# Kernel tuning notes

Hardware: AMD Instinct MI355X
Metric: run time of the kernel (lower is better)

Reference implementation:

```python
import jax, jax.numpy as jnp
import numpy as np

D_MODEL = 512
BINS = 64


def setup_inputs() -> dict:
    key = jax.random.key(0)
    ks = jax.random.split(key, 5)
    x = jax.random.normal(ks[0], (1, 512, D_MODEL), dtype=jnp.float32)
    # torch Linear(2d, d): weight [d, 2d]; store transposed [2d, d] for x @ W
    s1 = 1.0 / np.sqrt(2 * D_MODEL)
    W1 = jax.random.uniform(ks[1], (2 * D_MODEL, D_MODEL), jnp.float32, -s1, s1)
    b1 = jax.random.uniform(ks[2], (D_MODEL,), jnp.float32, -s1, s1)
    s2 = 1.0 / np.sqrt(D_MODEL)
    W2 = jax.random.uniform(ks[3], (D_MODEL, BINS), jnp.float32, -s2, s2)
    b2 = jax.random.uniform(ks[4], (BINS,), jnp.float32, -s2, s2)
    return {"x": x, "W1": W1, "b1": b1, "W2": W2, "b2": b2}


def reference(x, W1, b1, W2, b2):
    # pair = cat([xi, xj], -1); Linear(cat) == xi @ W1[:d] + xj @ W1[d:]
    # This factorization is exact and avoids materializing the [B,N,N,2d] tensor.
    d = x.shape[-1]
    hi = jnp.einsum('bnd,de->bne', x, W1[:d])      # [B, N, d]
    hj = jnp.einsum('bnd,de->bne', x, W1[d:])      # [B, N, d]
    h = hi[:, :, None, :] + hj[:, None, :, :] + b1  # [B, N, N, d]
    h = jax.nn.gelu(h, approximate=False)           # torch nn.GELU default is exact
    return jnp.einsum('bijd,de->bije', h, W2) + b2  # [B, N, N, bins]
```

## Files before the change

### kernel.cpp

```cpp
#include <hip/hip_runtime.h>
#include <hip/hip_fp16.h>

#define D 512
#define NTOK 512
#define BINS 64

typedef float v4f __attribute__((ext_vector_type(4)));
typedef int v4i __attribute__((ext_vector_type(4)));
typedef short short8 __attribute__((ext_vector_type(8)));
typedef _Float16 h8 __attribute__((ext_vector_type(8)));
typedef _Float16 h4 __attribute__((ext_vector_type(4)));

__device__ __forceinline__ __half2 gelu2(__half2 x) {
    __half2 a = __builtin_bit_cast(__half2, __builtin_bit_cast(int, x) & 0x7fff7fff);
    __half2 s = __hmul2(a, a);
    __half2 m = __hfma2(s, __float2half2_rn(-0.1029437f),
                           __float2half2_rn(-2.3022082f));
    __half2 q = __hmul2(a, m);
    __half2 e = h2exp2(q);
    __half2 n = __hfma2(e, __float2half2_rn(0.228584f),  __float2half2_rn(-0.675920f));
    n = __hfma2(e, n, __float2half2_rn(0.946902f));
    n = __hfma2(e, n, __float2half2_rn(-0.998521f));
    __half2 p = __hfma2(e, n, __float2half2_rn(1.0f));
    __half2 xneg = __hmul2(__hsub2(x, a), __float2half2_rn(0.5f));
    return __hfma2(a, p, xneg);
}

__device__ __forceinline__ __half2 bc_h2(int v) { return __builtin_bit_cast(__half2, v); }
__device__ __forceinline__ int bc_i(__half2 v) { return __builtin_bit_cast(int, v); }

__device__ __forceinline__ v4i pack8(v4f a, v4f b) {
    h8 o;
    o[0] = (_Float16)a.x; o[1] = (_Float16)a.y; o[2] = (_Float16)a.z; o[3] = (_Float16)a.w;
    o[4] = (_Float16)b.x; o[5] = (_Float16)b.y; o[6] = (_Float16)b.z; o[7] = (_Float16)b.w;
    return __builtin_bit_cast(v4i, o);
}

__global__ __launch_bounds__(256) void k_pack(const float* __restrict__ x,
                                              const float* __restrict__ W1,
                                              const float* __restrict__ W2,
                                              v4i* __restrict__ Ap,
                                              v4i* __restrict__ Wp,
                                              short8* __restrict__ Bp) {
    const int b = blockIdx.x;
    const int t = threadIdx.x;
    if (b < 32) {
        const int rb = b;
#pragma unroll
        for (int u = 0; u < 4; ++u) {
            const int e = t + 256 * u;
            const int l = e & 63, ks = e >> 6;
            const float* src = x + (size_t)(rb * 16 + (l & 15)) * D + ks * 32 + (l >> 4) * 8;
            v4f a = *(const v4f*)src;
            v4f c = *(const v4f*)(src + 4);
            Ap[(size_t)(rb * 16 + ks) * 64 + l] = pack8(a, c);
        }
    } else if (b < 288) {
        const int slot = (b - 32) * 256 + t;
        const int l = slot & 63;
        const int ks = (slot >> 6) & 15;
        const int nb = slot >> 10;
        const int ng = nb * 16 + (l & 15);
        const float* src = W1 + (size_t)((ng >> 9) * D + ks * 32 + (l >> 4) * 8) * D
                              + (ng & 511);
        h8 o;
#pragma unroll
        for (int j = 0; j < 8; ++j) o[j] = (_Float16)src[(size_t)j * D];
        Wp[(size_t)(nb * 16 + ks) * 64 + l] = __builtin_bit_cast(v4i, o);
    } else {
        const int tid = (b - 288) * 256 + t;
        const int ll = tid & 63;
        const int nt = (tid >> 6) & 3;
        const int kt = tid >> 8;
        const int colp = nt * 16 + (ll & 15);
        const int krow = kt * 32 + (ll >> 4) * 8;
        short8 v;
#pragma unroll
        for (int u = 0; u < 8; ++u) {
            _Float16 hv = (_Float16)W2[(size_t)(krow + u) * BINS + colp];
            v[u] = __builtin_bit_cast(short, hv);
        }
        Bp[tid] = v;
    }
}

__global__ __launch_bounds__(256) void k_gemm(const v4i* __restrict__ Ap,
                                              const v4i* __restrict__ Wp,
                                              const float* __restrict__ b1,
                                              _Float16* __restrict__ hi,
                                              _Float16* __restrict__ hj) {
    const int l = threadIdx.x & 63;
    const int w = threadIdx.x >> 6;
    const int c = l & 15;
    const int q = l >> 4;
    const int mb = blockIdx.x >> 4;
    const int cb = blockIdx.x & 15;
    const int nb = cb * 4 + w;

    const v4i* ap = Ap + (size_t)mb * 16 * 64 + l;
    const v4i* wp = Wp + (size_t)nb * 16 * 64 + l;

    v4f acc = {0.f, 0.f, 0.f, 0.f};
#pragma unroll 4
    for (int ks = 0; ks < 16; ++ks) {
        v4i a0 = ap[ks * 64];
        v4i bb = wp[ks * 64];
        acc = __builtin_amdgcn_mfma_f32_16x16x32_f16(__builtin_bit_cast(h8, a0),
                                                     __builtin_bit_cast(h8, bb), acc, 0, 0, 0);
    }

    const int ng = nb * 16 + c;
    const float b1v = (ng < D) ? b1[ng] : 0.0f;
    _Float16* dst = (ng < D ? hi : hj) + (ng & 511);
    const int row0 = mb * 16 + q * 4;
#pragma unroll
    for (int r = 0; r < 4; ++r)
        dst[(size_t)(row0 + r) * D] = (_Float16)(acc[r] + b1v);
}

__global__ __launch_bounds__(256, 6) void k_main(const __half* __restrict__ hi,
                                                 const __half* __restrict__ hj,
                                                 const v4i* __restrict__ Bp,
                                                 const float* __restrict__ b2,
                                                 float* __restrict__ out) {
    const int l = threadIdx.x & 63;
    const int w = threadIdx.x >> 6;
    const int c = l & 15;
    const int q = l >> 4;
    const int ib = (blockIdx.x >> 5) * 8;
    const int j0 = (blockIdx.x & 31) * 16;

    const __half* hjp = hj + (size_t)(j0 + c) * D + q * 8;
    const __half* hip = hi + (size_t)(ib + w * 2) * D + q * 8;
    const v4i* bp = Bp + l;

    v4f acc[2][4] = {};

    for (int kt = 0; kt < 16; ++kt) {
        const int ko = kt * 32;
        v4i hjraw = *(const v4i*)(hjp + ko);
        __half2 j0h = bc_h2(hjraw.x), j1h = bc_h2(hjraw.y);
        __half2 j2h = bc_h2(hjraw.z), j3h = bc_h2(hjraw.w);
        v4i bfr[4];
#pragma unroll
        for (int nt = 0; nt < 4; ++nt)
            bfr[nt] = bp[(kt * 4 + nt) * 64];
#pragma unroll
        for (int p = 0; p < 2; ++p) {
            v4i ar = *(const v4i*)(hip + (size_t)p * D + ko);
            __half2 g0 = gelu2(__hadd2(bc_h2(ar.x), j0h));
            __half2 g1 = gelu2(__hadd2(bc_h2(ar.y), j1h));
            __half2 g2 = gelu2(__hadd2(bc_h2(ar.z), j2h));
            __half2 g3 = gelu2(__hadd2(bc_h2(ar.w), j3h));
            v4i ai = {bc_i(g0), bc_i(g1), bc_i(g2), bc_i(g3)};
            h8 af = __builtin_bit_cast(h8, ai);
#pragma unroll
            for (int nt = 0; nt < 4; ++nt)
                acc[p][nt] = __builtin_amdgcn_mfma_f32_16x16x32_f16(
                    af, __builtin_bit_cast(h8, bfr[nt]), acc[p][nt], 0, 0, 0);
        }
    }

    const int i0 = ib + w * 2;
#pragma unroll
    for (int p = 0; p < 2; ++p) {
        const size_t rowbase = ((size_t)(i0 + p) * NTOK + j0 + q * 4) * BINS;
#pragma unroll
        for (int nt = 0; nt < 4; ++nt) {
            const float bb = b2[nt * 16 + c];
            float* op = out + rowbase + nt * 16 + c;
#pragma unroll
            for (int rr = 0; rr < 4; ++rr)
                op[(size_t)rr * BINS] = acc[p][nt][rr] + bb;
        }
    }
}

extern "C" void kernel_launch(void* const* d_in, const int* in_sizes, int n_in,
                              void* d_out, int out_size, void* d_ws, size_t ws_size,
                              hipStream_t stream) {
    const float* x  = (const float*)d_in[0];
    const float* W1 = (const float*)d_in[1];
    const float* b1 = (const float*)d_in[2];
    const float* W2 = (const float*)d_in[3];
    const float* b2 = (const float*)d_in[4];
    float* out = (float*)d_out;

    char* ws = (char*)d_ws;
    __half* hi = (__half*)ws;
    __half* hj = (__half*)(ws + (512u << 10));
    short8* Bp = (short8*)(ws + (1u << 20));
    v4i*    Ap = (v4i*)(ws + (1u << 20) + (64u << 10));
    v4i*    Wp = (v4i*)(ws + (1u << 20) + (64u << 10) + (512u << 10));

    k_pack<<<304, 256, 0, stream>>>(x, W1, W2, Ap, Wp, Bp);
    k_gemm<<<512, 256, 0, stream>>>(Ap, Wp, b1, (_Float16*)hi, (_Float16*)hj);
    k_main<<<2048, 256, 0, stream>>>(hi, hj, (const v4i*)Bp, b2, out);
}
```

Before: 132.1 us.

## Fuse pack and GEMM kernels, software-pipeline loads in main kernel

The separate fp16 packing kernel and the projection GEMM kernel are merged into one prep kernel. It reads x and W1 directly as fp32 and converts them in registers, while extra blocks pack W2. This removes one launch and the intermediate packed buffers. The main kernel now double-buffers its hj, hi and W2 fragment loads one k-step ahead, fully unrolls the loop, and lowers the launch-bounds occupancy hint from 6 to 3 to leave room for more registers. Risks are strided, uncoalesced W1 reads inside the GEMM and lower occupancy in the main kernel.

```diff
diff --git a/kernel.cpp b/kernel.cpp
--- a/kernel.cpp
+++ b/kernel.cpp
@@ -29,46 +29,17 @@
 __device__ __forceinline__ __half2 bc_h2(int v) { return __builtin_bit_cast(__half2, v); }
 __device__ __forceinline__ int bc_i(__half2 v) { return __builtin_bit_cast(int, v); }
 
-__device__ __forceinline__ v4i pack8(v4f a, v4f b) {
-    h8 o;
-    o[0] = (_Float16)a.x; o[1] = (_Float16)a.y; o[2] = (_Float16)a.z; o[3] = (_Float16)a.w;
-    o[4] = (_Float16)b.x; o[5] = (_Float16)b.y; o[6] = (_Float16)b.z; o[7] = (_Float16)b.w;
-    return __builtin_bit_cast(v4i, o);
-}
-
-__global__ __launch_bounds__(256) void k_pack(const float* __restrict__ x,
+__global__ __launch_bounds__(256) void k_prep(const float* __restrict__ x,
                                               const float* __restrict__ W1,
+                                              const float* __restrict__ b1,
                                               const float* __restrict__ W2,
-                                              v4i* __restrict__ Ap,
-                                              v4i* __restrict__ Wp,
+                                              _Float16* __restrict__ hi,
+                                              _Float16* __restrict__ hj,
                                               short8* __restrict__ Bp) {
     const int b = blockIdx.x;
     const int t = threadIdx.x;
-    if (b < 32) {
-        const int rb = b;
-#pragma unroll
-        for (int u = 0; u < 4; ++u) {
-            const int e = t + 256 * u;
-            const int l = e & 63, ks = e >> 6;
-            const float* src = x + (size_t)(rb * 16 + (l & 15)) * D + ks * 32 + (l >> 4) * 8;
-            v4f a = *(const v4f*)src;
-            v4f c = *(const v4f*)(src + 4);
-            Ap[(size_t)(rb * 16 + ks) * 64 + l] = pack8(a, c);
-        }
-    } else if (b < 288) {
-        const int slot = (b - 32) * 256 + t;
-        const int l = slot & 63;
-        const int ks = (slot >> 6) & 15;
-        const int nb = slot >> 10;
-        const int ng = nb * 16 + (l & 15);
-        const float* src = W1 + (size_t)((ng >> 9) * D + ks * 32 + (l >> 4) * 8) * D
-                              + (ng & 511);
-        h8 o;
-#pragma unroll
-        for (int j = 0; j < 8; ++j) o[j] = (_Float16)src[(size_t)j * D];
-        Wp[(size_t)(nb * 16 + ks) * 64 + l] = __builtin_bit_cast(v4i, o);
-    } else {
-        const int tid = (b - 288) * 256 + t;
+    if (b >= 512) {
+        const int tid = (b - 512) * 256 + t;
         const int ll = tid & 63;
         const int nt = (tid >> 6) & 3;
         const int kt = tid >> 8;
@@ -81,35 +52,37 @@
             v[u] = __builtin_bit_cast(short, hv);
         }
         Bp[tid] = v;
+        return;
     }
-}
-
-__global__ __launch_bounds__(256) void k_gemm(const v4i* __restrict__ Ap,
-                                              const v4i* __restrict__ Wp,
-                                              const float* __restrict__ b1,
-                                              _Float16* __restrict__ hi,
-                                              _Float16* __restrict__ hj) {
-    const int l = threadIdx.x & 63;
-    const int w = threadIdx.x >> 6;
+    const int l = t & 63;
+    const int w = t >> 6;
     const int c = l & 15;
     const int q = l >> 4;
-    const int mb = blockIdx.x >> 4;
-    const int cb = blockIdx.x & 15;
+    const int mb = b >> 4;
+    const int cb = b & 15;
     const int nb = cb * 4 + w;
+    const int ng = nb * 16 + c;
 
-    const v4i* ap = Ap + (size_t)mb * 16 * 64 + l;
-    const v4i* wp = Wp + (size_t)nb * 16 * 64 + l;
+    const float* xa = x + (size_t)(mb * 16 + c) * D + q * 8;
+    const float* wsrc = W1 + (size_t)((ng >> 9) * D + q * 8) * D + (ng & 511);
 
     v4f acc = {0.f, 0.f, 0.f, 0.f};
 #pragma unroll 4
     for (int ks = 0; ks < 16; ++ks) {
-        v4i a0 = ap[ks * 64];
-        v4i bb = wp[ks * 64];
-        acc = __builtin_amdgcn_mfma_f32_16x16x32_f16(__builtin_bit_cast(h8, a0),
-                                                     __builtin_bit_cast(h8, bb), acc, 0, 0, 0);
+        v4f a0 = *(const v4f*)(xa + ks * 32);
+        v4f a1 = *(const v4f*)(xa + ks * 32 + 4);
+        h8 af;
+        af[0] = (_Float16)a0.x; af[1] = (_Float16)a0.y;
+        af[2] = (_Float16)a0.z; af[3] = (_Float16)a0.w;
+        af[4] = (_Float16)a1.x; af[5] = (_Float16)a1.y;
+        af[6] = (_Float16)a1.z; af[7] = (_Float16)a1.w;
+        h8 bf;
+#pragma unroll
+        for (int j = 0; j < 8; ++j)
+            bf[j] = (_Float16)wsrc[(size_t)(ks * 32 + j) * D];
+        acc = __builtin_amdgcn_mfma_f32_16x16x32_f16(af, bf, acc, 0, 0, 0);
     }
 
-    const int ng = nb * 16 + c;
     const float b1v = (ng < D) ? b1[ng] : 0.0f;
     _Float16* dst = (ng < D ? hi : hj) + (ng & 511);
     const int row0 = mb * 16 + q * 4;
@@ -118,7 +91,7 @@
         dst[(size_t)(row0 + r) * D] = (_Float16)(acc[r] + b1v);
 }
 
-__global__ __launch_bounds__(256, 6) void k_main(const __half* __restrict__ hi,
+__global__ __launch_bounds__(256, 3) void k_main(const __half* __restrict__ hi,
                                                  const __half* __restrict__ hj,
                                                  const v4i* __restrict__ Bp,
                                                  const float* __restrict__ b2,
@@ -136,28 +109,43 @@
 
     v4f acc[2][4] = {};
 
+    v4i hjr[2];
+    v4i bfr[2][4];
+    v4i ar[2][2];
+    hjr[0] = *(const v4i*)hjp;
+#pragma unroll
+    for (int nt = 0; nt < 4; ++nt) bfr[0][nt] = bp[nt * 64];
+#pragma unroll
+    for (int p = 0; p < 2; ++p) ar[0][p] = *(const v4i*)(hip + (size_t)p * D);
+
+#pragma unroll
     for (int kt = 0; kt < 16; ++kt) {
-        const int ko = kt * 32;
-        v4i hjraw = *(const v4i*)(hjp + ko);
-        __half2 j0h = bc_h2(hjraw.x), j1h = bc_h2(hjraw.y);
-        __half2 j2h = bc_h2(hjraw.z), j3h = bc_h2(hjraw.w);
-        v4i bfr[4];
+        const int cur = kt & 1, nxt = cur ^ 1;
+        if (kt < 15) {
+            const int ko = (kt + 1) * 32;
+            hjr[nxt] = *(const v4i*)(hjp + ko);
 #pragma unroll
-        for (int nt = 0; nt < 4; ++nt)
-            bfr[nt] = bp[(kt * 4 + nt) * 64];
+            for (int nt = 0; nt < 4; ++nt)
+                bfr[nxt][nt] = bp[((kt + 1) * 4 + nt) * 64];
+#pragma unroll
+            for (int p = 0; p < 2; ++p)
+                ar[nxt][p] = *(const v4i*)(hip + (size_t)p * D + ko);
+        }
+        __half2 j0h = bc_h2(hjr[cur].x), j1h = bc_h2(hjr[cur].y);
+        __half2 j2h = bc_h2(hjr[cur].z), j3h = bc_h2(hjr[cur].w);
 #pragma unroll
         for (int p = 0; p < 2; ++p) {
-            v4i ar = *(const v4i*)(hip + (size_t)p * D + ko);
-            __half2 g0 = gelu2(__hadd2(bc_h2(ar.x), j0h));
-            __half2 g1 = gelu2(__hadd2(bc_h2(ar.y), j1h));
-            __half2 g2 = gelu2(__hadd2(bc_h2(ar.z), j2h));
-            __half2 g3 = gelu2(__hadd2(bc_h2(ar.w), j3h));
+            v4i arr = ar[cur][p];
+            __half2 g0 = gelu2(__hadd2(bc_h2(arr.x), j0h));
+            __half2 g1 = gelu2(__hadd2(bc_h2(arr.y), j1h));
+            __half2 g2 = gelu2(__hadd2(bc_h2(arr.z), j2h));
+            __half2 g3 = gelu2(__hadd2(bc_h2(arr.w), j3h));
             v4i ai = {bc_i(g0), bc_i(g1), bc_i(g2), bc_i(g3)};
             h8 af = __builtin_bit_cast(h8, ai);
 #pragma unroll
             for (int nt = 0; nt < 4; ++nt)
                 acc[p][nt] = __builtin_amdgcn_mfma_f32_16x16x32_f16(
-                    af, __builtin_bit_cast(h8, bfr[nt]), acc[p][nt], 0, 0, 0);
+                    af, __builtin_bit_cast(h8, bfr[cur][nt]), acc[p][nt], 0, 0, 0);
         }
     }
 
@@ -190,10 +178,7 @@
     __half* hi = (__half*)ws;
     __half* hj = (__half*)(ws + (512u << 10));
     short8* Bp = (short8*)(ws + (1u << 20));
-    v4i*    Ap = (v4i*)(ws + (1u << 20) + (64u << 10));
-    v4i*    Wp = (v4i*)(ws + (1u << 20) + (64u << 10) + (512u << 10));
 
-    k_pack<<<304, 256, 0, stream>>>(x, W1, W2, Ap, Wp, Bp);
-    k_gemm<<<512, 256, 0, stream>>>(Ap, Wp, b1, (_Float16*)hi, (_Float16*)hj);
+    k_prep<<<528, 256, 0, stream>>>(x, W1, b1, W2, (_Float16*)hi, (_Float16*)hj, Bp);
     k_main<<<2048, 256, 0, stream>>>(hi, hj, (const v4i*)Bp, b2, out);
 }
```

Result: no change. 133.8 us (+1.3%).
